# Kernel optimization log

Hardware: AMD Instinct MI355X
Metric: run time of the kernel (lower is better)

The kernel has to match this reference:

```python
import jax, jax.numpy as jnp
import numpy as np

EMBED_DIM = 1024
HEAD_SIZE = 64
B, T = 8, 2048


def setup_inputs() -> dict:
    key = jax.random.key(0)
    kx, kk, kq, kv = jax.random.split(key, 4)
    s = EMBED_DIM ** -0.5  # linear init scale (arbitrary for baseline)
    return {
        "x": jax.random.normal(kx, (B, T, EMBED_DIM), dtype=jnp.float32),
        "Wk": jax.random.normal(kk, (EMBED_DIM, HEAD_SIZE), dtype=jnp.float32) * s,
        "Wq": jax.random.normal(kq, (EMBED_DIM, HEAD_SIZE), dtype=jnp.float32) * s,
        "Wv": jax.random.normal(kv, (EMBED_DIM, HEAD_SIZE), dtype=jnp.float32) * s,
    }


def reference(x, Wk, Wq, Wv):
    # x: [B, T, C]; projections: [C, H]
    k = jnp.einsum("btc,ch->bth", x, Wk)
    q = jnp.einsum("btc,ch->bth", x, Wq)
    v = jnp.einsum("btc,ch->bth", x, Wv)
    Tlen = x.shape[1]
    scores = jnp.einsum("bqh,bkh->bqk", q, k) * (Wk.shape[1] ** -0.5)  # [B,T,T]
    causal = jnp.tril(jnp.ones((Tlen, Tlen), dtype=bool))
    scores = jnp.where(causal, scores, -jnp.inf)
    weights = jax.nn.softmax(scores, axis=-1)  # dropout=0 (eval mode)
    return jnp.einsum("bqk,bkh->bqh", weights, v)
```

## Files before the change

### kernel.cpp

```cpp
#include <hip/hip_runtime.h>
#include <hip/hip_bf16.h>


typedef __attribute__((ext_vector_type(8))) __bf16 bf16x8;
typedef __attribute__((ext_vector_type(4))) float f32x4;

#define BT   16384
#define TLEN 2048
#define NB   8

__device__ __forceinline__ ushort f2bf(float f) {
    __hip_bfloat16 h = __float2bfloat16(f);
    return __builtin_bit_cast(ushort, h);
}

__global__ void wtrans_kernel(const float* __restrict__ Wk, const float* __restrict__ Wq,
                              const float* __restrict__ Wv, ushort* __restrict__ wtb) {
    int idx = blockIdx.x * 256 + threadIdx.x;
    int e   = idx * 4;
    int s   = e >> 16;
    int rem = e & 65535;
    int k   = rem >> 6;
    int h   = rem & 63;
    const float* W = (s == 0) ? Wk : (s == 1) ? Wq : Wv;
    float sc = (s == 1) ? 0.125f : 1.0f;
    float4 v = *reinterpret_cast<const float4*>(&W[(size_t)k * 64 + h]);
    wtb[(size_t)(s * 64 + h + 0) * 1024 + k] = f2bf(v.x * sc);
    wtb[(size_t)(s * 64 + h + 1) * 1024 + k] = f2bf(v.y * sc);
    wtb[(size_t)(s * 64 + h + 2) * 1024 + k] = f2bf(v.z * sc);
    wtb[(size_t)(s * 64 + h + 3) * 1024 + k] = f2bf(v.w * sc);
}

__global__ __launch_bounds__(256, 2) void qkv_kernel3(
    const float* __restrict__ x, const ushort* __restrict__ wtb, ushort* __restrict__ kqv)
{
    __shared__ __align__(16) f32x4 red[2][24][64];

    const int tid  = threadIdx.x;
    const int lane = tid & 63;
    const int h    = tid >> 6;
    const int m    = lane & 15;
    const int g    = lane >> 4;
    const int R0   = blockIdx.x * 32;

    f32x4 acc[24];
    #pragma unroll
    for (int i = 0; i < 24; ++i) acc[i] = (f32x4){0.f, 0.f, 0.f, 0.f};

    const float*  xp0 = &x[(size_t)(R0 + m)      * 1024 + h * 256 + g * 8];
    const float*  xp1 = &x[(size_t)(R0 + 16 + m) * 1024 + h * 256 + g * 8];
    const ushort* wb  = &wtb[(size_t)m * 1024 + h * 256 + g * 8];

    float4 xa0a = *reinterpret_cast<const float4*>(xp0);
    float4 xa0b = *reinterpret_cast<const float4*>(xp0 + 4);
    float4 xa1a = *reinterpret_cast<const float4*>(xp1);
    float4 xa1b = *reinterpret_cast<const float4*>(xp1 + 4);

    #pragma unroll
    for (int st = 0; st < 8; ++st) {
        float4 xn0a, xn0b, xn1a, xn1b;
        if (st < 7) {
            xn0a = *reinterpret_cast<const float4*>(xp0 + (st + 1) * 32);
            xn0b = *reinterpret_cast<const float4*>(xp0 + (st + 1) * 32 + 4);
            xn1a = *reinterpret_cast<const float4*>(xp1 + (st + 1) * 32);
            xn1b = *reinterpret_cast<const float4*>(xp1 + (st + 1) * 32 + 4);
        }
        union { ushort u[8]; bf16x8 v; } a0, a1;
        a0.u[0] = f2bf(xa0a.x); a0.u[1] = f2bf(xa0a.y); a0.u[2] = f2bf(xa0a.z); a0.u[3] = f2bf(xa0a.w);
        a0.u[4] = f2bf(xa0b.x); a0.u[5] = f2bf(xa0b.y); a0.u[6] = f2bf(xa0b.z); a0.u[7] = f2bf(xa0b.w);
        a1.u[0] = f2bf(xa1a.x); a1.u[1] = f2bf(xa1a.y); a1.u[2] = f2bf(xa1a.z); a1.u[3] = f2bf(xa1a.w);
        a1.u[4] = f2bf(xa1b.x); a1.u[5] = f2bf(xa1b.y); a1.u[6] = f2bf(xa1b.z); a1.u[7] = f2bf(xa1b.w);
        #pragma unroll
        for (int nt = 0; nt < 12; ++nt) {
            bf16x8 b = *reinterpret_cast<const bf16x8*>(wb + (size_t)nt * 16 * 1024 + st * 32);
            acc[nt]      = __builtin_amdgcn_mfma_f32_16x16x32_bf16(a0.v, b, acc[nt],      0, 0, 0);
            acc[12 + nt] = __builtin_amdgcn_mfma_f32_16x16x32_bf16(a1.v, b, acc[12 + nt], 0, 0, 0);
        }
        xa0a = xn0a; xa0b = xn0b; xa1a = xn1a; xa1b = xn1b;
    }

    if (h == 1 || h == 3) {
        #pragma unroll
        for (int i = 0; i < 24; ++i) red[h >> 1][i][lane] = acc[i];
    }
    __syncthreads();
    if (h == 0 || h == 2) {
        #pragma unroll
        for (int i = 0; i < 24; ++i) acc[i] += red[h >> 1][i][lane];
    }
    __syncthreads();
    if (h == 2) {
        #pragma unroll
        for (int i = 0; i < 24; ++i) red[0][i][lane] = acc[i];
    }
    __syncthreads();
    if (h == 0) {
        #pragma unroll
        for (int f = 0; f < 2; ++f) {
            #pragma unroll
            for (int nt = 0; nt < 12; ++nt) {
                f32x4 a = acc[f * 12 + nt] + red[0][f * 12 + nt][lane];
                int s = nt >> 2;
                int c = (nt & 3) * 16 + m;
                #pragma unroll
                for (int j = 0; j < 4; ++j) {
                    size_t row = (size_t)R0 + f * 16 + g * 4 + j;
                    kqv[((size_t)s * BT + row) * 64 + c] = f2bf(a[j]);
                }
            }
        }
    }
}

__global__ __launch_bounds__(512) void attn_kernel2(
    const ushort* __restrict__ qs, const ushort* __restrict__ ks,
    const ushort* __restrict__ vs, float* __restrict__ out)
{
    __shared__ __align__(16) ushort kt[2][64][72];
    __shared__ __align__(16) ushort vt[2][64][72];
    __shared__ __align__(16) ushort pl[8][16][72];

    const int bid = blockIdx.x;
    const int wg  = (bid & 7) * 32 + (bid >> 3);
    const int qt  = wg & 31;
    const int b   = wg >> 5;

    const int tid  = threadIdx.x;
    const int lane = tid & 63;
    const int wv   = tid >> 6;
    const int wq   = wv & 3;
    const int hf   = wv >> 2;
    const int m    = lane & 15;
    const int g    = lane >> 4;
    const int ko   = g * 8;
    const int rowb = g * 4;
    const size_t base = (size_t)b * TLEN;

    bf16x8 qa[2];
    {
        size_t row_g = base + (size_t)qt * 64 + wq * 16 + m;
        qa[0] = *reinterpret_cast<const bf16x8*>(&qs[row_g * 64 + 0 + ko]);
        qa[1] = *reinterpret_cast<const bf16x8*>(&qs[row_g * 64 + 32 + ko]);
    }

    f32x4 o[4];
    #pragma unroll
    for (int nt = 0; nt < 4; ++nt) o[nt] = (f32x4){0.f, 0.f, 0.f, 0.f};
    float mrun[4] = {-1e30f, -1e30f, -1e30f, -1e30f};
    float lrun[4] = {0.f, 0.f, 0.f, 0.f};

    const int hs   = tid >> 8;
    const int seg  = (tid & 255) & 3;
    const int srow = (tid & 255) >> 2;

    const int nit = (qt >> 1) + 1;
    for (int it = 0; it < nit; ++it) {
        int ts = 2 * it + hs;
        if (ts <= qt) {
            const ushort* ksrc = &ks[(base + (size_t)ts * 64 + srow) * 64 + seg * 16];
            *reinterpret_cast<uint4*>(&kt[hs][srow][seg * 16 + 0]) = *reinterpret_cast<const uint4*>(ksrc);
            *reinterpret_cast<uint4*>(&kt[hs][srow][seg * 16 + 8]) = *reinterpret_cast<const uint4*>(ksrc + 8);
            const ushort* vsrc = &vs[(base + (size_t)ts * 64 + srow) * 64 + seg * 16];
            union { uint4 v[2]; ushort u[16]; } tv;
            tv.v[0] = *reinterpret_cast<const uint4*>(vsrc);
            tv.v[1] = *reinterpret_cast<const uint4*>(vsrc + 8);
            #pragma unroll
            for (int i = 0; i < 16; ++i) vt[hs][seg * 16 + i][srow] = tv.u[i];
        }
        __syncthreads();

        int t = 2 * it + hf;
        if (t <= qt) {
            f32x4 s[4];
            #pragma unroll
            for (int nt = 0; nt < 4; ++nt) s[nt] = (f32x4){0.f, 0.f, 0.f, 0.f};
            #pragma unroll
            for (int kk = 0; kk < 2; ++kk) {
                #pragma unroll
                for (int nt = 0; nt < 4; ++nt) {
                    bf16x8 bb = *reinterpret_cast<const bf16x8*>(&kt[hf][nt * 16 + m][kk * 32 + ko]);
                    s[nt] = __builtin_amdgcn_mfma_f32_16x16x32_bf16(qa[kk], bb, s[nt], 0, 0, 0);
                }
            }
            if (t == qt) {
                #pragma unroll
                for (int nt = 0; nt < 4; ++nt)
                    #pragma unroll
                    for (int j = 0; j < 4; ++j)
                        if (nt * 16 + m > wq * 16 + rowb + j) s[nt][j] = -1e30f;
            }
            #pragma unroll
            for (int j = 0; j < 4; ++j) {
                float mx = fmaxf(fmaxf(s[0][j], s[1][j]), fmaxf(s[2][j], s[3][j]));
                #pragma unroll
                for (int d = 1; d < 16; d <<= 1) mx = fmaxf(mx, __shfl_xor(mx, d, 64));
                float mnew = fmaxf(mrun[j], mx);
                float corr = __expf(mrun[j] - mnew);
                mrun[j] = mnew;
                float p0 = __expf(s[0][j] - mnew);
                float p1 = __expf(s[1][j] - mnew);
                float p2 = __expf(s[2][j] - mnew);
                float p3 = __expf(s[3][j] - mnew);
                float ps = p0 + p1 + p2 + p3;
                #pragma unroll
                for (int d = 1; d < 16; d <<= 1) ps += __shfl_xor(ps, d, 64);
                lrun[j] = lrun[j] * corr + ps;
                #pragma unroll
                for (int nt = 0; nt < 4; ++nt) o[nt][j] *= corr;
                pl[wv][rowb + j][0 * 16 + m] = f2bf(p0);
                pl[wv][rowb + j][1 * 16 + m] = f2bf(p1);
                pl[wv][rowb + j][2 * 16 + m] = f2bf(p2);
                pl[wv][rowb + j][3 * 16 + m] = f2bf(p3);
            }
            asm volatile("s_waitcnt lgkmcnt(0)" ::: "memory");
            __builtin_amdgcn_sched_barrier(0);
            #pragma unroll
            for (int kk = 0; kk < 2; ++kk) {
                bf16x8 pa = *reinterpret_cast<const bf16x8*>(&pl[wv][m][kk * 32 + ko]);
                #pragma unroll
                for (int nt = 0; nt < 4; ++nt) {
                    bf16x8 vb = *reinterpret_cast<const bf16x8*>(&vt[hf][nt * 16 + m][kk * 32 + ko]);
                    o[nt] = __builtin_amdgcn_mfma_f32_16x16x32_bf16(pa, vb, o[nt], 0, 0, 0);
                }
            }
        }
        __syncthreads();
    }

    float* mg = reinterpret_cast<float*>(&kt[0][0][0]);
    float* st = reinterpret_cast<float*>(&vt[0][0][0]);
    if (hf == 1) {
        #pragma unroll
        for (int nt = 0; nt < 4; ++nt)
            *reinterpret_cast<f32x4*>(&mg[((wq * 4 + nt) * 64 + lane) * 4]) = o[nt];
        if (m == 0) {
            #pragma unroll
            for (int j = 0; j < 4; ++j) {
                st[(wq * 16 + rowb + j) * 2 + 0] = mrun[j];
                st[(wq * 16 + rowb + j) * 2 + 1] = lrun[j];
            }
        }
    }
    __syncthreads();
    if (hf == 0) {
        float ea[4], eb[4], li[4];
        #pragma unroll
        for (int j = 0; j < 4; ++j) {
            float m1 = st[(wq * 16 + rowb + j) * 2 + 0];
            float l1 = st[(wq * 16 + rowb + j) * 2 + 1];
            float mm = fmaxf(mrun[j], m1);
            ea[j] = __expf(mrun[j] - mm);
            eb[j] = __expf(m1 - mm);
            li[j] = 1.0f / (lrun[j] * ea[j] + l1 * eb[j]);
        }
        #pragma unroll
        for (int nt = 0; nt < 4; ++nt) {
            f32x4 ob = *reinterpret_cast<const f32x4*>(&mg[((wq * 4 + nt) * 64 + lane) * 4]);
            #pragma unroll
            for (int j = 0; j < 4; ++j) {
                size_t rrow = base + (size_t)qt * 64 + wq * 16 + rowb + j;
                out[rrow * 64 + nt * 16 + m] = (o[nt][j] * ea[j] + ob[j] * eb[j]) * li[j];
            }
        }
    }
}

extern "C" void kernel_launch(void* const* d_in, const int* in_sizes, int n_in,
                              void* d_out, int out_size, void* d_ws, size_t ws_size,
                              hipStream_t stream) {
    const float* x  = (const float*)d_in[0];
    const float* Wk = (const float*)d_in[1];
    const float* Wq = (const float*)d_in[2];
    const float* Wv = (const float*)d_in[3];
    float* out = (float*)d_out;

    ushort* ws   = (ushort*)d_ws;
    ushort* kqv  = ws;
    ushort* kbuf = ws;
    ushort* qbuf = ws + (size_t)BT * 64;
    ushort* vbuf = ws + (size_t)2 * BT * 64;
    ushort* wtb  = ws + (size_t)3 * BT * 64;

    wtrans_kernel<<<dim3(192), 256, 0, stream>>>(Wk, Wq, Wv, wtb);
    qkv_kernel3<<<dim3(512), 256, 0, stream>>>(x, wtb, kqv);
    attn_kernel2<<<dim3(256), 512, 0, stream>>>(qbuf, kbuf, vbuf, out);
}
```

Before: 167.2 us.

## Store V transposed from projection, shrink tiles, reorder attention blocks longest-first

The projection kernel now handles 16 rows per block instead of 32, launches twice as many blocks at higher occupancy, and writes V in a transposed [64][BT] layout. The attention kernel no longer transposes V through scalar LDS stores. It copies K and V^T tiles with vector stores into padded shared memory. Attention blocks now cover 32 query rows with 4 waves, and heavy causal tiles are scheduled first to balance load. The risks are strided scalar global writes when storing V^T and extra redundant K/V loads across the smaller query tiles.

```diff
diff --git a/kernel.cpp b/kernel.cpp
--- a/kernel.cpp
+++ b/kernel.cpp
@@ -31,114 +31,106 @@
     wtb[(size_t)(s * 64 + h + 3) * 1024 + k] = f2bf(v.w * sc);
 }
 
-__global__ __launch_bounds__(256, 2) void qkv_kernel3(
-    const float* __restrict__ x, const ushort* __restrict__ wtb, ushort* __restrict__ kqv)
+__global__ __launch_bounds__(256, 4) void qkv_kernel4(
+    const float* __restrict__ x, const ushort* __restrict__ wtb,
+    ushort* __restrict__ kqv, ushort* __restrict__ vT)
 {
-    __shared__ __align__(16) f32x4 red[2][24][64];
+    __shared__ __align__(16) f32x4 red[2][12][64];
 
     const int tid  = threadIdx.x;
     const int lane = tid & 63;
     const int h    = tid >> 6;
     const int m    = lane & 15;
     const int g    = lane >> 4;
-    const int R0   = blockIdx.x * 32;
-
-    f32x4 acc[24];
+    const int R0   = blockIdx.x * 16;
+
+    f32x4 acc[12];
     #pragma unroll
-    for (int i = 0; i < 24; ++i) acc[i] = (f32x4){0.f, 0.f, 0.f, 0.f};
-
-    const float*  xp0 = &x[(size_t)(R0 + m)      * 1024 + h * 256 + g * 8];
-    const float*  xp1 = &x[(size_t)(R0 + 16 + m) * 1024 + h * 256 + g * 8];
-    const ushort* wb  = &wtb[(size_t)m * 1024 + h * 256 + g * 8];
-
-    float4 xa0a = *reinterpret_cast<const float4*>(xp0);
-    float4 xa0b = *reinterpret_cast<const float4*>(xp0 + 4);
-    float4 xa1a = *reinterpret_cast<const float4*>(xp1);
-    float4 xa1b = *reinterpret_cast<const float4*>(xp1 + 4);
+    for (int i = 0; i < 12; ++i) acc[i] = (f32x4){0.f, 0.f, 0.f, 0.f};
+
+    const float*  xp = &x[(size_t)(R0 + m) * 1024 + h * 256 + g * 8];
+    const ushort* wb = &wtb[(size_t)m * 1024 + h * 256 + g * 8];
+
+    float4 xa = *reinterpret_cast<const float4*>(xp);
+    float4 xb = *reinterpret_cast<const float4*>(xp + 4);
 
     #pragma unroll
     for (int st = 0; st < 8; ++st) {
-        float4 xn0a, xn0b, xn1a, xn1b;
+        float4 xna, xnb;
         if (st < 7) {
-            xn0a = *reinterpret_cast<const float4*>(xp0 + (st + 1) * 32);
-            xn0b = *reinterpret_cast<const float4*>(xp0 + (st + 1) * 32 + 4);
-            xn1a = *reinterpret_cast<const float4*>(xp1 + (st + 1) * 32);
-            xn1b = *reinterpret_cast<const float4*>(xp1 + (st + 1) * 32 + 4);
-        }
-        union { ushort u[8]; bf16x8 v; } a0, a1;
-        a0.u[0] = f2bf(xa0a.x); a0.u[1] = f2bf(xa0a.y); a0.u[2] = f2bf(xa0a.z); a0.u[3] = f2bf(xa0a.w);
-        a0.u[4] = f2bf(xa0b.x); a0.u[5] = f2bf(xa0b.y); a0.u[6] = f2bf(xa0b.z); a0.u[7] = f2bf(xa0b.w);
-        a1.u[0] = f2bf(xa1a.x); a1.u[1] = f2bf(xa1a.y); a1.u[2] = f2bf(xa1a.z); a1.u[3] = f2bf(xa1a.w);
-        a1.u[4] = f2bf(xa1b.x); a1.u[5] = f2bf(xa1b.y); a1.u[6] = f2bf(xa1b.z); a1.u[7] = f2bf(xa1b.w);
+            xna = *reinterpret_cast<const float4*>(xp + (st + 1) * 32);
+            xnb = *reinterpret_cast<const float4*>(xp + (st + 1) * 32 + 4);
+        }
+        union { ushort u[8]; bf16x8 v; } av;
+        av.u[0] = f2bf(xa.x); av.u[1] = f2bf(xa.y); av.u[2] = f2bf(xa.z); av.u[3] = f2bf(xa.w);
+        av.u[4] = f2bf(xb.x); av.u[5] = f2bf(xb.y); av.u[6] = f2bf(xb.z); av.u[7] = f2bf(xb.w);
         #pragma unroll
         for (int nt = 0; nt < 12; ++nt) {
             bf16x8 b = *reinterpret_cast<const bf16x8*>(wb + (size_t)nt * 16 * 1024 + st * 32);
-            acc[nt]      = __builtin_amdgcn_mfma_f32_16x16x32_bf16(a0.v, b, acc[nt],      0, 0, 0);
-            acc[12 + nt] = __builtin_amdgcn_mfma_f32_16x16x32_bf16(a1.v, b, acc[12 + nt], 0, 0, 0);
-        }
-        xa0a = xn0a; xa0b = xn0b; xa1a = xn1a; xa1b = xn1b;
+            acc[nt] = __builtin_amdgcn_mfma_f32_16x16x32_bf16(av.v, b, acc[nt], 0, 0, 0);
+        }
+        xa = xna; xb = xnb;
     }
 
     if (h == 1 || h == 3) {
         #pragma unroll
-        for (int i = 0; i < 24; ++i) red[h >> 1][i][lane] = acc[i];
+        for (int i = 0; i < 12; ++i) red[h >> 1][i][lane] = acc[i];
     }
     __syncthreads();
     if (h == 0 || h == 2) {
         #pragma unroll
-        for (int i = 0; i < 24; ++i) acc[i] += red[h >> 1][i][lane];
+        for (int i = 0; i < 12; ++i) acc[i] += red[h >> 1][i][lane];
     }
     __syncthreads();
     if (h == 2) {
         #pragma unroll
-        for (int i = 0; i < 24; ++i) red[0][i][lane] = acc[i];
+        for (int i = 0; i < 12; ++i) red[0][i][lane] = acc[i];
     }
     __syncthreads();
     if (h == 0) {
         #pragma unroll
-        for (int f = 0; f < 2; ++f) {
-            #pragma unroll
-            for (int nt = 0; nt < 12; ++nt) {
-                f32x4 a = acc[f * 12 + nt] + red[0][f * 12 + nt][lane];
-                int s = nt >> 2;
-                int c = (nt & 3) * 16 + m;
-                #pragma unroll
-                for (int j = 0; j < 4; ++j) {
-                    size_t row = (size_t)R0 + f * 16 + g * 4 + j;
-                    kqv[((size_t)s * BT + row) * 64 + c] = f2bf(a[j]);
-                }
-            }
-        }
-    }
-}
-
-__global__ __launch_bounds__(512) void attn_kernel2(
+        for (int nt = 0; nt < 12; ++nt) {
+            f32x4 a = acc[nt] + red[0][nt][lane];
+            int s = nt >> 2;
+            int c = (nt & 3) * 16 + m;
+            #pragma unroll
+            for (int j = 0; j < 4; ++j) {
+                size_t row = (size_t)R0 + g * 4 + j;
+                if (s < 2) kqv[((size_t)s * BT + row) * 64 + c] = f2bf(a[j]);
+                else       vT[(size_t)c * BT + row]            = f2bf(a[j]);
+            }
+        }
+    }
+}
+
+__global__ __launch_bounds__(256, 3) void attn_kernel3(
     const ushort* __restrict__ qs, const ushort* __restrict__ ks,
-    const ushort* __restrict__ vs, float* __restrict__ out)
+    const ushort* __restrict__ vT, float* __restrict__ out)
 {
-    __shared__ __align__(16) ushort kt[2][64][72];
-    __shared__ __align__(16) ushort vt[2][64][72];
-    __shared__ __align__(16) ushort pl[8][16][72];
+    __shared__ __align__(16) ushort kt[2][64][80];
+    __shared__ __align__(16) ushort vt[2][64][80];
+    __shared__ __align__(16) ushort pl[4][16][72];
 
     const int bid = blockIdx.x;
-    const int wg  = (bid & 7) * 32 + (bid >> 3);
-    const int qt  = wg & 31;
-    const int b   = wg >> 5;
+    const int i   = 63 - (bid >> 3);
+    const int b   = bid & 7;
+    const int Ti  = (i >> 1) + 1;
 
     const int tid  = threadIdx.x;
     const int lane = tid & 63;
     const int wv   = tid >> 6;
-    const int wq   = wv & 3;
-    const int hf   = wv >> 2;
+    const int wq   = wv & 1;
+    const int hf   = wv >> 1;
     const int m    = lane & 15;
     const int g    = lane >> 4;
     const int ko   = g * 8;
     const int rowb = g * 4;
     const size_t base = (size_t)b * TLEN;
+    const int qr0 = i * 32 + wq * 16;
 
     bf16x8 qa[2];
     {
-        size_t row_g = base + (size_t)qt * 64 + wq * 16 + m;
+        size_t row_g = base + qr0 + m;
         qa[0] = *reinterpret_cast<const bf16x8*>(&qs[row_g * 64 + 0 + ko]);
         qa[1] = *reinterpret_cast<const bf16x8*>(&qs[row_g * 64 + 32 + ko]);
     }
@@ -149,28 +141,28 @@
     float mrun[4] = {-1e30f, -1e30f, -1e30f, -1e30f};
     float lrun[4] = {0.f, 0.f, 0.f, 0.f};
 
-    const int hs   = tid >> 8;
-    const int seg  = (tid & 255) & 3;
-    const int srow = (tid & 255) >> 2;
-
-    const int nit = (qt >> 1) + 1;
+    const int hs2 = tid >> 7;
+    const int tl  = tid & 127;
+    const int sr  = tl >> 1;
+    const int sh  = (tl & 1) * 32;
+
+    const int nit = (Ti + 1) >> 1;
     for (int it = 0; it < nit; ++it) {
-        int ts = 2 * it + hs;
-        if (ts <= qt) {
-            const ushort* ksrc = &ks[(base + (size_t)ts * 64 + srow) * 64 + seg * 16];
-            *reinterpret_cast<uint4*>(&kt[hs][srow][seg * 16 + 0]) = *reinterpret_cast<const uint4*>(ksrc);
-            *reinterpret_cast<uint4*>(&kt[hs][srow][seg * 16 + 8]) = *reinterpret_cast<const uint4*>(ksrc + 8);
-            const ushort* vsrc = &vs[(base + (size_t)ts * 64 + srow) * 64 + seg * 16];
-            union { uint4 v[2]; ushort u[16]; } tv;
-            tv.v[0] = *reinterpret_cast<const uint4*>(vsrc);
-            tv.v[1] = *reinterpret_cast<const uint4*>(vsrc + 8);
-            #pragma unroll
-            for (int i = 0; i < 16; ++i) vt[hs][seg * 16 + i][srow] = tv.u[i];
+        int ts = 2 * it + hs2;
+        if (ts < Ti) {
+            const ushort* ksrc = &ks[(base + (size_t)ts * 64 + sr) * 64 + sh];
+            uint4* kdst = reinterpret_cast<uint4*>(&kt[hs2][sr][sh]);
+            #pragma unroll
+            for (int q = 0; q < 4; ++q) kdst[q] = reinterpret_cast<const uint4*>(ksrc)[q];
+            const ushort* vsrc = &vT[(size_t)sr * BT + base + (size_t)ts * 64 + sh];
+            uint4* vdst = reinterpret_cast<uint4*>(&vt[hs2][sr][sh]);
+            #pragma unroll
+            for (int q = 0; q < 4; ++q) vdst[q] = reinterpret_cast<const uint4*>(vsrc)[q];
         }
         __syncthreads();
 
         int t = 2 * it + hf;
-        if (t <= qt) {
+        if (t < Ti) {
             f32x4 s[4];
             #pragma unroll
             for (int nt = 0; nt < 4; ++nt) s[nt] = (f32x4){0.f, 0.f, 0.f, 0.f};
@@ -182,12 +174,12 @@
                     s[nt] = __builtin_amdgcn_mfma_f32_16x16x32_bf16(qa[kk], bb, s[nt], 0, 0, 0);
                 }
             }
-            if (t == qt) {
+            if (t == Ti - 1) {
                 #pragma unroll
                 for (int nt = 0; nt < 4; ++nt)
                     #pragma unroll
                     for (int j = 0; j < 4; ++j)
-                        if (nt * 16 + m > wq * 16 + rowb + j) s[nt][j] = -1e30f;
+                        if (t * 64 + nt * 16 + m > qr0 + rowb + j) s[nt][j] = -1e30f;
             }
             #pragma unroll
             for (int j = 0; j < 4; ++j) {
@@ -258,7 +250,7 @@
             f32x4 ob = *reinterpret_cast<const f32x4*>(&mg[((wq * 4 + nt) * 64 + lane) * 4]);
             #pragma unroll
             for (int j = 0; j < 4; ++j) {
-                size_t rrow = base + (size_t)qt * 64 + wq * 16 + rowb + j;
+                size_t rrow = base + qr0 + rowb + j;
                 out[rrow * 64 + nt * 16 + m] = (o[nt][j] * ea[j] + ob[j] * eb[j]) * li[j];
             }
         }
@@ -278,10 +270,10 @@
     ushort* kqv  = ws;
     ushort* kbuf = ws;
     ushort* qbuf = ws + (size_t)BT * 64;
-    ushort* vbuf = ws + (size_t)2 * BT * 64;
+    ushort* vTb  = ws + (size_t)2 * BT * 64;
     ushort* wtb  = ws + (size_t)3 * BT * 64;
 
     wtrans_kernel<<<dim3(192), 256, 0, stream>>>(Wk, Wq, Wv, wtb);
-    qkv_kernel3<<<dim3(512), 256, 0, stream>>>(x, wtb, kqv);
-    attn_kernel2<<<dim3(256), 512, 0, stream>>>(qbuf, kbuf, vbuf, out);
-}
+    qkv_kernel4<<<dim3(1024), 256, 0, stream>>>(x, wtb, kqv, vTb);
+    attn_kernel3<<<dim3(512), 256, 0, stream>>>(qbuf, kbuf, vTb, out);
+}
```

After: 176.5 us. +5.6%, slower.
